# Kernel optimization log

Hardware: AMD Instinct MI355X
Metric: run time of the kernel (lower is better)

The kernel has to match this reference:

```python
import jax, jax.numpy as jnp
import numpy as np

S = 64       # n_subdomains
N = 131072   # n_points
D = 2        # in_dim (t, x)
H = 32       # hidden
SCALE, SHIFT = 1.0, 0.0  # unnorm_para


def setup_inputs() -> dict:
    key = jax.random.key(0)
    ks = jax.random.split(key, 10)
    # --- subdomain geometry: tile x in [-1,1] into S overlapping cells, t spans [0,1]
    edges = np.linspace(-1.0, 1.0, S + 1)
    cell = edges[1] - edges[0]
    lo_core = np.stack([np.zeros(S), edges[:-1]], axis=1)   # (S,2) = [t_lo, x_lo]
    hi_core = np.stack([np.ones(S), edges[1:]], axis=1)
    lo_ext = lo_core - np.array([0.1, 0.3 * cell])
    hi_ext = hi_core + np.array([0.1, 0.3 * cell])
    # --- collocation points: t ~ U[0,1], x ~ U[-1,1]
    u01 = jax.random.uniform(ks[0], (N, D), dtype=jnp.float32)
    x = u01 * jnp.array([1.0, 2.0], jnp.float32) + jnp.array([0.0, -1.0], jnp.float32)
    # --- stacked per-subdomain MLP params (in->H, H->H, H->H, H->1), tanh activations
    def init(k, shape, fan_in):
        return (jax.random.normal(k, shape, dtype=jnp.float32) / np.sqrt(fan_in)).astype(jnp.float32)
    return {
        "x": x,
        "lo_core": jnp.asarray(lo_core, jnp.float32),
        "hi_core": jnp.asarray(hi_core, jnp.float32),
        "lo_ext": jnp.asarray(lo_ext, jnp.float32),
        "hi_ext": jnp.asarray(hi_ext, jnp.float32),
        "W_in": init(ks[1], (S, H, D), D),
        "b_in": jnp.zeros((S, H), jnp.float32),
        "W_h1": init(ks[2], (S, H, H), H),
        "b_h1": jnp.zeros((S, H), jnp.float32),
        "W_h2": init(ks[3], (S, H, H), H),
        "b_h2": jnp.zeros((S, H), jnp.float32),
        "W_out": init(ks[4], (S, 1, H), H),
        "b_out": jnp.zeros((S, 1), jnp.float32),
    }


def reference(x, lo_core, hi_core, lo_ext, hi_ext,
              W_in, b_in, W_h1, b_h1, W_h2, b_h2, W_out, b_out):
    # 1) per-subdomain normalization of x to [-1,1]:  (S,N,D)
    center = (lo_ext + hi_ext) * 0.5
    half_w = (hi_ext - lo_ext) * 0.5
    xn = (x[None, :, :] - center[:, None, :]) / half_w[:, None, :]
    # 2) all tiny subnet MLPs evaluated in one batched pass (vmap equivalent)
    h = jnp.tanh(jnp.einsum('snd,shd->snh', xn, W_in) + b_in[:, None, :])
    h = jnp.tanh(jnp.einsum('snh,skh->snk', h, W_h1) + b_h1[:, None, :])
    h = jnp.tanh(jnp.einsum('snh,skh->snk', h, W_h2) + b_h2[:, None, :])
    out = jnp.einsum('snh,soh->sno', h, W_out) + b_out[:, None, :]   # (S,N,1)
    out = out * SCALE + SHIFT  # unnorm
    # 3) sigmoid-product window per subdomain: (S,N,1)
    overlap = jnp.maximum(hi_ext - hi_core, lo_core - lo_ext)       # (S,D)
    width = hi_ext - lo_ext
    s = 4.0 / (2.0 * overlap * width + 1e-8)                        # (S,D)
    left = jax.nn.sigmoid(s[:, None, :] * (x[None, :, :] - lo_core[:, None, :]))
    right = jax.nn.sigmoid(s[:, None, :] * (hi_core[:, None, :] - x[None, :, :]))
    w = jnp.prod(left * right, axis=-1, keepdims=True)              # (S,N,1)
    w = w / (jnp.sum(w, axis=0, keepdims=True) + 1e-8)
    # 4) weighted sum across subdomains
    u = jnp.sum(out * w, axis=0)                                    # (N,1)
    # 5) hard BC constraint: -sin(pi*x) + tanh(x+1)tanh(x-1)tanh(t)*u
    g = -jnp.sin(jnp.pi * x[:, 1])[:, None]
    factor = (jnp.tanh(x[:, 1] + 1.0) * jnp.tanh(x[:, 1] - 1.0) * jnp.tanh(x[:, 0]))[:, None]
    return g + factor * u
```

## Files before the change

### kernel.cpp

```cpp
#include <hip/hip_runtime.h>
#include <math.h>

namespace {
constexpr int S = 64;
constexpr int NP = 131072;
constexpr int H = 32;
constexpr int BLK = 256;
constexpr int NBK = 3 * S;
constexpr int NBH = 64;
constexpr int PPB = NP / NBH;
constexpr int WPB = 4;
constexpr int CHUNK = 64;
constexpr int NCG = 9;

typedef float v2f __attribute__((ext_vector_type(2)));

constexpr int WS_OFF  = 0;
constexpr int WS_BH   = 194;
constexpr int WS_LIST = WS_BH + NBH * NBK;
constexpr int WS_XS   = WS_LIST + NP;
constexpr int WS_PART = WS_XS + 2 * NP;

__device__ __forceinline__ float dev_exp2(float v) {
    return __builtin_amdgcn_exp2f(v);
}
__device__ __forceinline__ float fast_tanh(float v) {
    float e = dev_exp2(v * 2.8853900817779268f);
    return 1.0f - __fdividef(2.0f, e + 1.0f);
}
__device__ __forceinline__ float fast_sigmoid(float z) {
    return __fdividef(1.0f, 1.0f + dev_exp2(z * -1.4426950408889634f));
}
__device__ __forceinline__ void cell_band(float xx, int& c, float& frac) {
    float pos = (xx + 1.0f) * 32.0f;
    c = min(S - 1, max(0, (int)floorf(pos)));
    frac = pos - (float)c;
}
__device__ __forceinline__ int band_of(float frac) {
    return (frac > 0.33f ? 1 : 0) + (frac > 0.67f ? 1 : 0);
}

__global__ __launch_bounds__(BLK) void k_hist(const float* __restrict__ x,
                                              int* __restrict__ blockhist) {
    __shared__ int lh[NBK];
    const int tid = threadIdx.x;
    if (tid < NBK) lh[tid] = 0;
    __syncthreads();
    const int pbase = blockIdx.x * PPB;
    for (int t = tid; t < PPB; t += BLK) {
        int c; float frac;
        cell_band(x[2 * (pbase + t) + 1], c, frac);
        atomicAdd(&lh[3 * c + band_of(frac)], 1);
    }
    __syncthreads();
    if (tid < NBK) blockhist[blockIdx.x * NBK + tid] = lh[tid];
}

__global__ __launch_bounds__(NBK) void k_scan(int* __restrict__ blockhist,
                                              int* __restrict__ off) {
    const int t = threadIdx.x;
    int tot = 0;
    for (int b = 0; b < NBH; ++b) tot += blockhist[b * NBK + t];
    int incl = tot;
    #pragma unroll
    for (int d = 1; d < 64; d <<= 1) {
        int o = __shfl_up(incl, d);
        if ((t & 63) >= d) incl += o;
    }
    __shared__ int wsum[3];
    if ((t & 63) == 63) wsum[t >> 6] = incl;
    __syncthreads();
    int pre = 0;
    for (int w = 0; w < (t >> 6); ++w) pre += wsum[w];
    const int o = pre + incl - tot;
    off[t] = o;
    if (t == NBK - 1) off[NBK] = pre + incl;
    int run = o;
    for (int b = 0; b < NBH; ++b) {
        int v = blockhist[b * NBK + t];
        blockhist[b * NBK + t] = run;
        run += v;
    }
}

__global__ __launch_bounds__(BLK) void k_scatter(const float* __restrict__ x,
                                                 const int* __restrict__ base,
                                                 int* __restrict__ list,
                                                 float2* __restrict__ xsorted) {
    __shared__ int lh[NBK];
    __shared__ int lbase[NBK];
    const int tid = threadIdx.x;
    if (tid < NBK) { lh[tid] = 0; lbase[tid] = base[blockIdx.x * NBK + tid]; }
    __syncthreads();
    const int pbase = blockIdx.x * PPB;
    for (int t = tid; t < PPB; t += BLK) {
        const int p = pbase + t;
        const float2 xv = ((const float2*)x)[p];
        int c; float frac;
        cell_band(xv.y, c, frac);
        const int k = 3 * c + band_of(frac);
        const int r = atomicAdd(&lh[k], 1);
        const int pos = lbase[k] + r;
        list[pos] = p;
        xsorted[pos] = xv;
    }
}

__global__ __launch_bounds__(256, 3) void k_main(
    const float2* __restrict__ xsorted,
    const float* __restrict__ lo_core, const float* __restrict__ hi_core,
    const float* __restrict__ lo_ext,  const float* __restrict__ hi_ext,
    const float* __restrict__ W_in,  const float* __restrict__ b_in,
    const float* __restrict__ W_h1,  const float* __restrict__ b_h1,
    const float* __restrict__ W_h2,  const float* __restrict__ b_h2,
    const float* __restrict__ W_out, const float* __restrict__ b_out,
    const int* __restrict__ off,
    float2* __restrict__ part)
{
    const int j = blockIdx.x;
    const int z = blockIdx.z;
    int lo, hi;
    if (z == 0)      { lo = off[3*j];     hi = off[3*j+3]; }
    else if (z == 1) { if (j + 1 >= S) return; lo = off[3*j+3]; hi = off[3*j+5]; }
    else             { if (j == 0)     return; lo = off[3*j-2]; hi = off[3*j]; }
    const int cnt = hi - lo;
    const int wid  = threadIdx.x >> 6;
    const int lane = threadIdx.x & 63;
    const int base = (blockIdx.y * WPB + wid) * CHUNK;
    if (base >= cnt) return;
    const int idx = base + lane;
    const bool act = idx < cnt;
    const int slot = lo + (act ? idx : cnt - 1);
    const float2 xv = xsorted[slot];
    const float tt = xv.x, xx = xv.y;

    const float le0 = lo_ext[2*j+0], he0 = hi_ext[2*j+0];
    const float le1 = lo_ext[2*j+1], he1 = hi_ext[2*j+1];
    const float ic0 = (le0 + he0) * 0.5f, ih0 = __fdividef(1.0f, (he0 - le0) * 0.5f);
    const float ic1 = (le1 + he1) * 0.5f, ih1 = __fdividef(1.0f, (he1 - le1) * 0.5f);
    const float xn0 = (tt - ic0) * ih0;
    const float xn1 = (xx - ic1) * ih1;
    const v2f xn = {xn0, xn1};

    v2f h0[H/2], h1[H/2];

    {
        const v2f* Wiv = (const v2f*)(W_in + j * (H * 2));
        const float* bi = b_in + j * H;
        #pragma unroll
        for (int k2 = 0; k2 < H/2; ++k2) {
            v2f aA = __builtin_elementwise_fma(xn, Wiv[2*k2+0], (v2f){bi[2*k2+0], 0.0f});
            v2f aB = __builtin_elementwise_fma(xn, Wiv[2*k2+1], (v2f){bi[2*k2+1], 0.0f});
            h0[k2] = (v2f){fast_tanh(aA.x + aA.y), fast_tanh(aB.x + aB.y)};
        }
    }
    {
        const v2f* W1v = (const v2f*)(W_h1 + j * (H * H));
        const float* b1 = b_h1 + j * H;
        #pragma unroll
        for (int k2 = 0; k2 < H/2; ++k2) {
            const v2f* rowA = W1v + (2*k2) * (H/2);
            const v2f* rowB = rowA + (H/2);
            v2f aA = {b1[2*k2+0], 0.0f};
            v2f aB = {b1[2*k2+1], 0.0f};
            #pragma unroll
            for (int q2 = 0; q2 < H/2; ++q2) {
                aA = __builtin_elementwise_fma(h0[q2], rowA[q2], aA);
                aB = __builtin_elementwise_fma(h0[q2], rowB[q2], aB);
            }
            h1[k2] = (v2f){fast_tanh(aA.x + aA.y), fast_tanh(aB.x + aB.y)};
        }
    }
    {
        const v2f* W2v = (const v2f*)(W_h2 + j * (H * H));
        const float* b2 = b_h2 + j * H;
        #pragma unroll
        for (int k2 = 0; k2 < H/2; ++k2) {
            const v2f* rowA = W2v + (2*k2) * (H/2);
            const v2f* rowB = rowA + (H/2);
            v2f aA = {b2[2*k2+0], 0.0f};
            v2f aB = {b2[2*k2+1], 0.0f};
            #pragma unroll
            for (int q2 = 0; q2 < H/2; ++q2) {
                aA = __builtin_elementwise_fma(h1[q2], rowA[q2], aA);
                aB = __builtin_elementwise_fma(h1[q2], rowB[q2], aB);
            }
            h0[k2] = (v2f){fast_tanh(aA.x + aA.y), fast_tanh(aB.x + aB.y)};
        }
    }
    float acc;
    {
        const v2f* Wov = (const v2f*)(W_out + j * H);
        v2f a = {b_out[j], 0.0f};
        #pragma unroll
        for (int q2 = 0; q2 < H/2; ++q2) {
            a = __builtin_elementwise_fma(h0[q2], Wov[q2], a);
        }
        acc = a.x + a.y;
    }

    float w = 1.0f;
    {
        const float lc = lo_core[2*j+0], hc = hi_core[2*j+0];
        const float ov = fmaxf(he0 - hc, lc - le0);
        const float sc = __fdividef(4.0f, fmaf(2.0f * ov, he0 - le0, 1e-8f));
        w *= fast_sigmoid(sc * (tt - lc)) * fast_sigmoid(sc * (hc - tt));
    }
    {
        const float lc = lo_core[2*j+1], hc = hi_core[2*j+1];
        const float ov = fmaxf(he1 - hc, lc - le1);
        const float sc = __fdividef(4.0f, fmaf(2.0f * ov, he1 - le1, 1e-8f));
        w *= fast_sigmoid(sc * (xx - lc)) * fast_sigmoid(sc * (hc - xx));
    }
    if (act) part[z * NP + slot] = make_float2(acc * w, w);
}

__global__ __launch_bounds__(BLK) void k_combine(
    const float2* __restrict__ part,
    const float2* __restrict__ xsorted,
    const int* __restrict__ list,
    float* __restrict__ out)
{
    const int i = blockIdx.x * BLK + threadIdx.x;
    const float2 xv = xsorted[i];
    const float tt = xv.x, xx = xv.y;
    int c; float frac;
    cell_band(xx, c, frac);
    float nsum = 0.0f, dsum = 0.0f;
    if (c > 0 && !(frac > 0.67f)) {
        const float2 p1 = part[NP + i];
        nsum = p1.x; dsum = p1.y;
    }
    const float2 p0 = part[i];
    nsum += p0.x; dsum += p0.y;
    if (c < S - 1 && frac > 0.33f) {
        const float2 p2 = part[2 * NP + i];
        nsum += p2.x; dsum += p2.y;
    }
    const float u = __fdividef(nsum, dsum + 1e-8f);
    const float g = -sinf(3.14159265358979323846f * xx);
    const float factor = fast_tanh(xx + 1.0f) * fast_tanh(xx - 1.0f) * fast_tanh(tt);
    out[list[i]] = fmaf(factor, u, g);
}
}

extern "C" void kernel_launch(void* const* d_in, const int* in_sizes, int n_in,
                              void* d_out, int out_size, void* d_ws, size_t ws_size,
                              hipStream_t stream) {
    const float* x       = (const float*)d_in[0];
    const float* lo_core = (const float*)d_in[1];
    const float* hi_core = (const float*)d_in[2];
    const float* lo_ext  = (const float*)d_in[3];
    const float* hi_ext  = (const float*)d_in[4];
    const float* W_in    = (const float*)d_in[5];
    const float* b_in    = (const float*)d_in[6];
    const float* W_h1    = (const float*)d_in[7];
    const float* b_h1    = (const float*)d_in[8];
    const float* W_h2    = (const float*)d_in[9];
    const float* b_h2    = (const float*)d_in[10];
    const float* W_out   = (const float*)d_in[11];
    const float* b_out   = (const float*)d_in[12];
    float* out = (float*)d_out;

    int* ws        = (int*)d_ws;
    int* off       = ws + WS_OFF;
    int* blockhist = ws + WS_BH;
    int* list      = ws + WS_LIST;
    float2* xsorted = (float2*)(ws + WS_XS);
    float2* part    = (float2*)(ws + WS_PART);

    hipLaunchKernelGGL(k_hist,    dim3(NBH),       dim3(BLK), 0, stream, x, blockhist);
    hipLaunchKernelGGL(k_scan,    dim3(1),         dim3(NBK), 0, stream, blockhist, off);
    hipLaunchKernelGGL(k_scatter, dim3(NBH),       dim3(BLK), 0, stream, x, blockhist, list, xsorted);
    hipLaunchKernelGGL(k_main,    dim3(S, NCG, 3), dim3(256), 0, stream,
        xsorted, lo_core, hi_core, lo_ext, hi_ext, W_in, b_in, W_h1, b_h1,
        W_h2, b_h2, W_out, b_out, off, part);
    hipLaunchKernelGGL(k_combine, dim3(NP / BLK),  dim3(BLK), 0, stream, part, xsorted, list, out);
}
```

Baseline: 59.02 us.

## Replace fixed 3D grid with compacted per-wave chunk descriptor list

The scan kernel now also builds a compacted list of 64-point chunk descriptors (slot start, length, subdomain, zone), one per wave of work. The main kernel launches a flat grid sized for the maximum chunk count and each wave reads its descriptor, so the fixed S x NCG x 3 grid and its many early-exiting empty waves go away. Launch bounds also rise to 4 blocks per CU. This adds a serial descriptor write loop in the single-block scan and relies on a fixed NCH_MAX bound on the chunk count.

```diff
diff --git a/kernel.cpp b/kernel.cpp
--- a/kernel.cpp
+++ b/kernel.cpp
@@ -10,16 +10,18 @@
 constexpr int NBH = 64;
 constexpr int PPB = NP / NBH;
 constexpr int WPB = 4;
-constexpr int CHUNK = 64;
-constexpr int NCG = 9;
+constexpr int NCH_MAX = 6400;
+constexpr int NMB = NCH_MAX / WPB;
 
 typedef float v2f __attribute__((ext_vector_type(2)));
 
 constexpr int WS_OFF  = 0;
+constexpr int WS_NCH  = 193;
 constexpr int WS_BH   = 194;
 constexpr int WS_LIST = WS_BH + NBH * NBK;
 constexpr int WS_XS   = WS_LIST + NP;
 constexpr int WS_PART = WS_XS + 2 * NP;
+constexpr int WS_DESC = WS_PART + 6 * NP;
 
 __device__ __forceinline__ float dev_exp2(float v) {
     return __builtin_amdgcn_exp2f(v);
@@ -57,7 +59,12 @@
 }
 
 __global__ __launch_bounds__(NBK) void k_scan(int* __restrict__ blockhist,
-                                              int* __restrict__ off) {
+                                              int* __restrict__ off,
+                                              int* __restrict__ nch,
+                                              int2* __restrict__ desc) {
+    __shared__ int loff[NBK + 1];
+    __shared__ int wsum[3];
+    __shared__ int wsum2[3];
     const int t = threadIdx.x;
     int tot = 0;
     for (int b = 0; b < NBH; ++b) tot += blockhist[b * NBK + t];
@@ -67,19 +74,45 @@
         int o = __shfl_up(incl, d);
         if ((t & 63) >= d) incl += o;
     }
-    __shared__ int wsum[3];
     if ((t & 63) == 63) wsum[t >> 6] = incl;
     __syncthreads();
     int pre = 0;
     for (int w = 0; w < (t >> 6); ++w) pre += wsum[w];
     const int o = pre + incl - tot;
-    off[t] = o;
-    if (t == NBK - 1) off[NBK] = pre + incl;
+    off[t] = o;  loff[t] = o;
+    if (t == NBK - 1) { off[NBK] = pre + incl; loff[NBK] = pre + incl; }
     int run = o;
     for (int b = 0; b < NBH; ++b) {
         int v = blockhist[b * NBK + t];
         blockhist[b * NBK + t] = run;
         run += v;
+    }
+    __syncthreads();
+
+    const int j = t / 3;
+    const int z = t - 3 * j;
+    int lo2 = 0, hi2 = 0;
+    if (z == 0)                { lo2 = loff[3*j];   hi2 = loff[3*j+3]; }
+    else if (z == 1 && j+1 < S){ lo2 = loff[3*j+3]; hi2 = loff[3*j+5]; }
+    else if (z == 2 && j > 0)  { lo2 = loff[3*j-2]; hi2 = loff[3*j]; }
+    const int cnt = hi2 - lo2;
+    const int cc  = (cnt + 63) >> 6;
+    int incl2 = cc;
+    #pragma unroll
+    for (int d = 1; d < 64; d <<= 1) {
+        int o2 = __shfl_up(incl2, d);
+        if ((t & 63) >= d) incl2 += o2;
+    }
+    if ((t & 63) == 63) wsum2[t >> 6] = incl2;
+    __syncthreads();
+    int pre2 = 0;
+    for (int w = 0; w < (t >> 6); ++w) pre2 += wsum2[w];
+    const int pos = pre2 + incl2 - cc;
+    if (t == NBK - 1) nch[0] = pre2 + incl2;
+    for (int i = 0; i < cc; ++i) {
+        const int rem = cnt - (i << 6);
+        const int len = rem < 64 ? rem : 64;
+        desc[pos + i] = make_int2(lo2 + (i << 6), len | (j << 8) | (z << 16));
     }
 }
 
@@ -106,7 +139,7 @@
     }
 }
 
-__global__ __launch_bounds__(256, 3) void k_main(
+__global__ __launch_bounds__(256, 4) void k_main(
     const float2* __restrict__ xsorted,
     const float* __restrict__ lo_core, const float* __restrict__ hi_core,
     const float* __restrict__ lo_ext,  const float* __restrict__ hi_ext,
@@ -114,23 +147,21 @@
     const float* __restrict__ W_h1,  const float* __restrict__ b_h1,
     const float* __restrict__ W_h2,  const float* __restrict__ b_h2,
     const float* __restrict__ W_out, const float* __restrict__ b_out,
-    const int* __restrict__ off,
+    const int* __restrict__ nch, const int2* __restrict__ desc,
     float2* __restrict__ part)
 {
-    const int j = blockIdx.x;
-    const int z = blockIdx.z;
-    int lo, hi;
-    if (z == 0)      { lo = off[3*j];     hi = off[3*j+3]; }
-    else if (z == 1) { if (j + 1 >= S) return; lo = off[3*j+3]; hi = off[3*j+5]; }
-    else             { if (j == 0)     return; lo = off[3*j-2]; hi = off[3*j]; }
-    const int cnt = hi - lo;
     const int wid  = threadIdx.x >> 6;
     const int lane = threadIdx.x & 63;
-    const int base = (blockIdx.y * WPB + wid) * CHUNK;
-    if (base >= cnt) return;
-    const int idx = base + lane;
-    const bool act = idx < cnt;
-    const int slot = lo + (act ? idx : cnt - 1);
+    const int w = blockIdx.x * WPB + wid;
+    if (w >= nch[0]) return;
+    const int2 d = desc[w];
+    const int slot0 = __builtin_amdgcn_readfirstlane(d.x);
+    const int meta  = __builtin_amdgcn_readfirstlane(d.y);
+    const int len = meta & 255;
+    const int j   = (meta >> 8) & 255;
+    const int z   = meta >> 16;
+    const bool act = lane < len;
+    const int slot = slot0 + (act ? lane : len - 1);
     const float2 xv = xsorted[slot];
     const float tt = xv.x, xx = xv.y;
 
@@ -138,9 +169,7 @@
     const float le1 = lo_ext[2*j+1], he1 = hi_ext[2*j+1];
     const float ic0 = (le0 + he0) * 0.5f, ih0 = __fdividef(1.0f, (he0 - le0) * 0.5f);
     const float ic1 = (le1 + he1) * 0.5f, ih1 = __fdividef(1.0f, (he1 - le1) * 0.5f);
-    const float xn0 = (tt - ic0) * ih0;
-    const float xn1 = (xx - ic1) * ih1;
-    const v2f xn = {xn0, xn1};
+    const v2f xn = {(tt - ic0) * ih0, (xx - ic1) * ih1};
 
     v2f h0[H/2], h1[H/2];
 
@@ -199,20 +228,20 @@
         acc = a.x + a.y;
     }
 
-    float w = 1.0f;
+    float w2 = 1.0f;
     {
         const float lc = lo_core[2*j+0], hc = hi_core[2*j+0];
         const float ov = fmaxf(he0 - hc, lc - le0);
         const float sc = __fdividef(4.0f, fmaf(2.0f * ov, he0 - le0, 1e-8f));
-        w *= fast_sigmoid(sc * (tt - lc)) * fast_sigmoid(sc * (hc - tt));
+        w2 *= fast_sigmoid(sc * (tt - lc)) * fast_sigmoid(sc * (hc - tt));
     }
     {
         const float lc = lo_core[2*j+1], hc = hi_core[2*j+1];
         const float ov = fmaxf(he1 - hc, lc - le1);
         const float sc = __fdividef(4.0f, fmaf(2.0f * ov, he1 - le1, 1e-8f));
-        w *= fast_sigmoid(sc * (xx - lc)) * fast_sigmoid(sc * (hc - xx));
-    }
-    if (act) part[z * NP + slot] = make_float2(acc * w, w);
+        w2 *= fast_sigmoid(sc * (xx - lc)) * fast_sigmoid(sc * (hc - xx));
+    }
+    if (act) part[z * NP + slot] = make_float2(acc * w2, w2);
 }
 
 __global__ __launch_bounds__(BLK) void k_combine(
@@ -264,16 +293,18 @@
 
     int* ws        = (int*)d_ws;
     int* off       = ws + WS_OFF;
+    int* nch       = ws + WS_NCH;
     int* blockhist = ws + WS_BH;
     int* list      = ws + WS_LIST;
     float2* xsorted = (float2*)(ws + WS_XS);
     float2* part    = (float2*)(ws + WS_PART);
-
-    hipLaunchKernelGGL(k_hist,    dim3(NBH),       dim3(BLK), 0, stream, x, blockhist);
-    hipLaunchKernelGGL(k_scan,    dim3(1),         dim3(NBK), 0, stream, blockhist, off);
-    hipLaunchKernelGGL(k_scatter, dim3(NBH),       dim3(BLK), 0, stream, x, blockhist, list, xsorted);
-    hipLaunchKernelGGL(k_main,    dim3(S, NCG, 3), dim3(256), 0, stream,
+    int2*   desc    = (int2*)(ws + WS_DESC);
+
+    hipLaunchKernelGGL(k_hist,    dim3(NBH),      dim3(BLK), 0, stream, x, blockhist);
+    hipLaunchKernelGGL(k_scan,    dim3(1),        dim3(NBK), 0, stream, blockhist, off, nch, desc);
+    hipLaunchKernelGGL(k_scatter, dim3(NBH),      dim3(BLK), 0, stream, x, blockhist, list, xsorted);
+    hipLaunchKernelGGL(k_main,    dim3(NMB),      dim3(256), 0, stream,
         xsorted, lo_core, hi_core, lo_ext, hi_ext, W_in, b_in, W_h1, b_h1,
-        W_h2, b_h2, W_out, b_out, off, part);
-    hipLaunchKernelGGL(k_combine, dim3(NP / BLK),  dim3(BLK), 0, stream, part, xsorted, list, out);
-}
+        W_h2, b_h2, W_out, b_out, nch, desc, part);
+    hipLaunchKernelGGL(k_combine, dim3(NP / BLK), dim3(BLK), 0, stream, part, xsorted, list, out);
+}
```

New measurement: 57.38 us. 2.8% less time.
